# Kernel tuning notes

Hardware: AMD Instinct MI355X
Metric: run time of the kernel (lower is better)

Reference implementation:

```python
import jax, jax.numpy as jnp
import numpy as np

_EPS = 1e-08
SEG = 1024
HOP = 256
PAD = SEG // 2

# periodic Hann window, matching torch.hann_window(SEG) (periodic=True default)
_WINDOW = 0.5 * (1.0 - np.cos(2.0 * np.pi * np.arange(SEG) / SEG))


def setup_inputs() -> dict:
    key = jax.random.key(0)
    k1, k2 = jax.random.split(key)
    B, T = 32, 480000
    estimate = jax.random.normal(k1, (B, T), dtype=jnp.float32)
    target = jax.random.normal(k2, (B, T), dtype=jnp.float32)
    return {"estimate": estimate, "target": target}


def _frame(x):
    # x: [B, T_padded] -> [B, n_frames, SEG] overlapping frames (hop=HOP)
    n_frames = (x.shape[1] - SEG) // HOP + 1
    idx = np.arange(n_frames)[:, None] * HOP + np.arange(SEG)[None, :]
    return x[:, idx]


def reference(estimate, target):
    # zero-mean per utterance
    tgt = target - jnp.mean(target, axis=1, keepdims=True)
    est = estimate - jnp.mean(estimate, axis=1, keepdims=True)
    # centering: reflect-pad SEG//2 on both sides
    tgt = jnp.pad(tgt, ((0, 0), (PAD, PAD)), mode="reflect")
    est = jnp.pad(est, ((0, 0), (PAD, PAD)), mode="reflect")
    # overlapping frames + Hann windowing
    w = jnp.asarray(_WINDOW, dtype=tgt.dtype)  # [SEG]
    T_f = _frame(tgt) * w  # [B, F, SEG]
    E_f = _frame(est) * w  # [B, F, SEG]
    # SI-SDR per segment
    dot = jnp.sum(E_f * T_f, axis=2, keepdims=True)
    s_target_energy = jnp.sum(T_f * T_f, axis=2, keepdims=True) + _EPS
    scaled_target = dot * T_f / s_target_energy
    e_noise = E_f - scaled_target
    ratio = jnp.sum(scaled_target * scaled_target, axis=2) / (
        jnp.sum(e_noise * e_noise, axis=2) + _EPS
    )
    losses = -10.0 * jnp.log10(ratio + _EPS)  # [B, F]
    return losses
```

## Files before the change

kernel.cpp:

```cpp
#include <hip/hip_runtime.h>

#define NB 32
#define TLEN 480000
#define NF 1876
#define FR 4
#define WPR 469
#define WTHREADS 256

template <int CTRL>
__device__ __forceinline__ float dpp_add(float x) {
    int y = __builtin_amdgcn_update_dpp(0, __float_as_int(x), CTRL, 0xF, 0xF, true);
    return x + __int_as_float(y);
}

__device__ __forceinline__ float wave_reduce(float s) {
    s = dpp_add<0xB1>(s);
    s = dpp_add<0x4E>(s);
    s = dpp_add<0x124>(s);
    s = dpp_add<0x128>(s);
    s += __shfl_xor(s, 16);
    s += __shfl_xor(s, 32);
    return s;
}

__device__ __forceinline__ float f4c(const float4& v, int j) {
    return j == 0 ? v.x : (j == 1 ? v.y : (j == 2 ? v.z : v.w));
}

__device__ __forceinline__ float w2fast(float p) {
    float w = 0.5f - 0.5f * __cosf(p * (6.28318530717958647692f / 1024.0f));
    return w * w;
}

__global__ __launch_bounds__(WTHREADS) void seg_frames(
    const float* __restrict__ est, const float* __restrict__ tgt,
    float* __restrict__ ws_part, float* __restrict__ ws_bs)
{
    const int tid  = threadIdx.x;
    const int lane = tid & 63;
    const int wave = tid >> 6;
    const int b    = blockIdx.y;
    const int wv   = blockIdx.x * 4 + wave;
    if (wv >= WPR) return;
    const int fb = wv * FR;

    const float* erow = est + (size_t)b * TLEN;
    const float* trow = tgt + (size_t)b * TLEN;

    float pe = 0.f, pt = 0.f;

    if (fb >= 4 && fb <= 1868) {
        const float4* e4 = (const float4*)erow;
        const float4* t4 = (const float4*)trow;

        float4 E[7], T[7];
#pragma unroll
        for (int m = 0; m < 7; ++m) {
            int g = 64 * (fb + m) - 128 + lane;
            E[m] = e4[g];
            T[m] = t4[g];
        }

        float w2v[4][4];
#pragma unroll
        for (int q = 0; q < 4; ++q)
#pragma unroll
            for (int j = 0; j < 4; ++j)
                w2v[q][j] = w2fast((float)(256 * q + 4 * lane + j));

        float acc[4][5];
#pragma unroll
        for (int i = 0; i < 4; ++i)
#pragma unroll
            for (int s5 = 0; s5 < 5; ++s5) acc[i][s5] = 0.f;

#pragma unroll
        for (int m = 0; m < 7; ++m) {
            float4 ev4 = E[m], tv4 = T[m];
#pragma unroll
            for (int j = 0; j < 4; ++j) {
                float e = f4c(ev4, j), t = f4c(tv4, j);
                float et = e * t, tt2 = t * t, ee2 = e * e;
#pragma unroll
                for (int i = 0; i < 4; ++i) {
                    if (m - i < 0 || m - i > 3) continue;
                    float w2 = w2v[m - i][j];
                    acc[i][0] = fmaf(w2, et,  acc[i][0]);
                    acc[i][1] = fmaf(w2, tt2, acc[i][1]);
                    acc[i][2] = fmaf(w2, ee2, acc[i][2]);
                    acc[i][3] = fmaf(w2, e,   acc[i][3]);
                    acc[i][4] = fmaf(w2, t,   acc[i][4]);
                }
            }
            if (m < 4) {
                pe += (ev4.x + ev4.y) + (ev4.z + ev4.w);
                pt += (tv4.x + tv4.y) + (tv4.z + tv4.w);
            }
        }

#pragma unroll
        for (int i = 0; i < 4; ++i) {
            float s0 = wave_reduce(acc[i][0]);
            float s1 = wave_reduce(acc[i][1]);
            float s2 = wave_reduce(acc[i][2]);
            float s3 = wave_reduce(acc[i][3]);
            float s4 = wave_reduce(acc[i][4]);
            if (lane == 0) {
                float* p = ws_part + (size_t)(b * NF + fb + i) * 5;
                p[0] = s0; p[1] = s1; p[2] = s2; p[3] = s3; p[4] = s4;
            }
        }
    } else {
        int nfr = NF - fb;
        if (nfr > FR) nfr = FR;

        float w2v[4][4];
#pragma unroll
        for (int q = 0; q < 4; ++q)
#pragma unroll
            for (int j = 0; j < 4; ++j)
                w2v[q][j] = w2fast((float)(256 * q + 4 * lane + j));

        for (int i = 0; i < nfr; ++i) {
            int f = fb + i;
            float s_et = 0.f, s_tt = 0.f, s_ee = 0.f, s_e = 0.f, s_t = 0.f;
#pragma unroll
            for (int q = 0; q < 4; ++q)
#pragma unroll
                for (int j = 0; j < 4; ++j) {
                    int s = 256 * f - 512 + 256 * q + 4 * lane + j;
                    int idx = s < 0 ? -s : (s >= TLEN ? 2 * (TLEN - 1) - s : s);
                    float ev = erow[idx], tv = trow[idx];
                    float w2 = w2v[q][j];
                    float et = ev * tv;
                    s_et = fmaf(w2, et,      s_et);
                    s_tt = fmaf(w2, tv * tv, s_tt);
                    s_ee = fmaf(w2, ev * ev, s_ee);
                    s_e  = fmaf(w2, ev, s_e);
                    s_t  = fmaf(w2, tv, s_t);
                }
            s_et = wave_reduce(s_et);
            s_tt = wave_reduce(s_tt);
            s_ee = wave_reduce(s_ee);
            s_e  = wave_reduce(s_e);
            s_t  = wave_reduce(s_t);
            if (lane == 0) {
                float* p = ws_part + (size_t)(b * NF + f) * 5;
                p[0] = s_et; p[1] = s_tt; p[2] = s_ee; p[3] = s_e; p[4] = s_t;
            }
        }

        const float4* e4 = (const float4*)erow;
        const float4* t4 = (const float4*)trow;
        if (fb == 0) {
#pragma unroll
            for (int k = 0; k < 2; ++k) {
                float4 ev4 = e4[lane + 64 * k];
                float4 tv4 = t4[lane + 64 * k];
                pe += (ev4.x + ev4.y) + (ev4.z + ev4.w);
                pt += (tv4.x + tv4.y) + (tv4.z + tv4.w);
            }
        } else {
#pragma unroll
            for (int k = 0; k < 5; ++k) {
                int g = 119680 + lane + 64 * k;
                float4 ev4 = e4[g];
                float4 tv4 = t4[g];
                pe += (ev4.x + ev4.y) + (ev4.z + ev4.w);
                pt += (tv4.x + tv4.y) + (tv4.z + tv4.w);
            }
        }
    }

    pe = wave_reduce(pe);
    pt = wave_reduce(pt);
    if (lane == 0) {
        ws_bs[(0 * NB + b) * WPR + wv] = pe;
        ws_bs[(1 * NB + b) * WPR + wv] = pt;
    }
}

__global__ __launch_bounds__(WTHREADS) void seg_final(
    const float* __restrict__ ws_part, const float* __restrict__ ws_bs,
    float* __restrict__ out)
{
    const int tid  = threadIdx.x;
    const int lane = tid & 63;
    const int wave = tid >> 6;
    const int idx0 = blockIdx.x * WTHREADS;

    int b0 = idx0 / NF;
    int ilast = idx0 + WTHREADS - 1;
    if (ilast > NB * NF - 1) ilast = NB * NF - 1;
    int b1 = ilast / NF;

    __shared__ float smean[4];
    {
        int sig = wave & 1;
        int row = (wave >> 1) ? b1 : b0;
        const float* pbs = ws_bs + (size_t)(sig * NB + row) * WPR;
        float s = 0.f;
        for (int c = lane; c < WPR; c += 64) s += pbs[c];
        s = wave_reduce(s);
        if (lane == 0) smean[wave] = s * (1.0f / (float)TLEN);
    }
    __syncthreads();

    int idx = idx0 + tid;
    if (idx >= NB * NF) return;
    int b = idx / NF;
    int which = (b == b0) ? 0 : 1;
    float me = smean[which * 2 + 0];
    float mt = smean[which * 2 + 1];

    const float* p = ws_part + (size_t)idx * 5;
    float S_et = p[0], S_tt = p[1], S_ee = p[2], S_e = p[3], S_t = p[4];
    const float W2 = 384.0f;

    float dot = S_et - mt * S_e - me * S_t + me * mt * W2;
    float tt  = S_tt - 2.0f * mt * S_t + mt * mt * W2;
    float ee  = S_ee - 2.0f * me * S_e + me * me * W2;

    float a     = dot / (tt + 1e-8f);
    float st2   = a * a * tt;
    float en2   = ee - 2.0f * a * dot + st2;
    float ratio = st2 / (en2 + 1e-8f);
    out[idx] = -10.0f * log10f(ratio + 1e-8f);
}

extern "C" void kernel_launch(void* const* d_in, const int* in_sizes, int n_in,
                              void* d_out, int out_size, void* d_ws, size_t ws_size,
                              hipStream_t stream)
{
    const float* est = (const float*)d_in[0];
    const float* tgt = (const float*)d_in[1];
    float* out = (float*)d_out;

    float* ws      = (float*)d_ws;
    float* ws_part = ws;
    float* ws_bs   = ws_part + (size_t)NB * NF * 5;

    dim3 grid1((WPR + 3) / 4, NB);
    seg_frames<<<grid1, WTHREADS, 0, stream>>>(est, tgt, ws_part, ws_bs);
    dim3 grid2((NB * NF + WTHREADS - 1) / WTHREADS);
    seg_final<<<grid2, WTHREADS, 0, stream>>>(ws_part, ws_bs, out);
}
```

Measured before the change: 35.95 us.

## Widen each wave to a 16-frame strip with rolling register reuse

Each wave now computes 16 consecutive frames instead of 4, holding an 11-slot rolling register buffer of float4 chunks. Each group of 4 frames reuses 7 chunks, and later chunks are loaded into slots that are no longer needed. This cuts redundant global loads of overlapping frame data from 7/4 to about 19/16 chunks per frame. Results are packed across lanes so lanes 0-4 write all 16 frames' partial sums, and launch bounds request 2 blocks per SM. The trade-off is fewer waves (118 per row), so there is less parallelism and more register pressure, and edge strips now cover 16 frames on the slow reflect path.

Result: slower. 44.89 us (+24.9%).

```diff
diff --git a/kernel.cpp b/kernel.cpp
--- a/kernel.cpp
+++ b/kernel.cpp
@@ -3,8 +3,8 @@
 #define NB 32
 #define TLEN 480000
 #define NF 1876
-#define FR 4
-#define WPR 469
+#define FSTRIP 16
+#define WPR 118
 #define WTHREADS 256
 
 template <int CTRL>
@@ -32,7 +32,7 @@
     return w * w;
 }
 
-__global__ __launch_bounds__(WTHREADS) void seg_frames(
+__global__ __launch_bounds__(WTHREADS, 2) void seg_frames(
     const float* __restrict__ est, const float* __restrict__ tgt,
     float* __restrict__ ws_part, float* __restrict__ ws_bs)
 {
@@ -42,23 +42,23 @@
     const int b    = blockIdx.y;
     const int wv   = blockIdx.x * 4 + wave;
     if (wv >= WPR) return;
-    const int fb = wv * FR;
+    const int fb = wv * FSTRIP;
 
     const float* erow = est + (size_t)b * TLEN;
     const float* trow = tgt + (size_t)b * TLEN;
 
     float pe = 0.f, pt = 0.f;
 
-    if (fb >= 4 && fb <= 1868) {
+    if (wv >= 1 && wv <= 116) {
         const float4* e4 = (const float4*)erow;
         const float4* t4 = (const float4*)trow;
-
-        float4 E[7], T[7];
-#pragma unroll
-        for (int m = 0; m < 7; ++m) {
-            int g = 64 * (fb + m) - 128 + lane;
-            E[m] = e4[g];
-            T[m] = t4[g];
+        const int gbase = 1024 * wv - 128 + lane;
+
+        float4 E[11], T[11];
+#pragma unroll
+        for (int m = 0; m < 11; ++m) {
+            E[m] = e4[gbase + 64 * m];
+            T[m] = t4[gbase + 64 * m];
         }
 
         float w2v[4][4];
@@ -68,51 +68,81 @@
             for (int j = 0; j < 4; ++j)
                 w2v[q][j] = w2fast((float)(256 * q + 4 * lane + j));
 
-        float acc[4][5];
-#pragma unroll
-        for (int i = 0; i < 4; ++i)
-#pragma unroll
-            for (int s5 = 0; s5 < 5; ++s5) acc[i][s5] = 0.f;
-
-#pragma unroll
-        for (int m = 0; m < 7; ++m) {
-            float4 ev4 = E[m], tv4 = T[m];
-#pragma unroll
-            for (int j = 0; j < 4; ++j) {
-                float e = f4c(ev4, j), t = f4c(tv4, j);
-                float et = e * t, tt2 = t * t, ee2 = e * e;
-#pragma unroll
-                for (int i = 0; i < 4; ++i) {
-                    if (m - i < 0 || m - i > 3) continue;
-                    float w2 = w2v[m - i][j];
-                    acc[i][0] = fmaf(w2, et,  acc[i][0]);
-                    acc[i][1] = fmaf(w2, tt2, acc[i][1]);
-                    acc[i][2] = fmaf(w2, ee2, acc[i][2]);
-                    acc[i][3] = fmaf(w2, e,   acc[i][3]);
-                    acc[i][4] = fmaf(w2, t,   acc[i][4]);
-                }
-            }
-            if (m < 4) {
-                pe += (ev4.x + ev4.y) + (ev4.z + ev4.w);
-                pt += (tv4.x + tv4.y) + (tv4.z + tv4.w);
-            }
-        }
-
-#pragma unroll
-        for (int i = 0; i < 4; ++i) {
-            float s0 = wave_reduce(acc[i][0]);
-            float s1 = wave_reduce(acc[i][1]);
-            float s2 = wave_reduce(acc[i][2]);
-            float s3 = wave_reduce(acc[i][3]);
-            float s4 = wave_reduce(acc[i][4]);
-            if (lane == 0) {
-                float* p = ws_part + (size_t)(b * NF + fb + i) * 5;
-                p[0] = s0; p[1] = s1; p[2] = s2; p[3] = s3; p[4] = s4;
-            }
+        float vres[FSTRIP];
+
+#pragma unroll
+        for (int gq = 0; gq < 4; ++gq) {
+            if (gq == 1) {
+#pragma unroll
+                for (int m = 11; m < 15; ++m) {
+                    E[m - 11] = e4[gbase + 64 * m];
+                    T[m - 11] = t4[gbase + 64 * m];
+                }
+            }
+            if (gq == 2) {
+#pragma unroll
+                for (int m = 15; m < 19; ++m) {
+                    E[m - 11] = e4[gbase + 64 * m];
+                    T[m - 11] = t4[gbase + 64 * m];
+                }
+            }
+
+            float acc[4][5];
+#pragma unroll
+            for (int i = 0; i < 4; ++i)
+#pragma unroll
+                for (int s5 = 0; s5 < 5; ++s5) acc[i][s5] = 0.f;
+
+#pragma unroll
+            for (int k = 0; k < 7; ++k) {
+                const int slot = (4 * gq + k) % 11;
+                float4 ev4 = E[slot], tv4 = T[slot];
+#pragma unroll
+                for (int j = 0; j < 4; ++j) {
+                    float e = f4c(ev4, j), t = f4c(tv4, j);
+                    float et = e * t, tt2 = t * t, ee2 = e * e;
+#pragma unroll
+                    for (int i = 0; i < 4; ++i) {
+                        if (k - i < 0 || k - i > 3) continue;
+                        float w2 = w2v[k - i][j];
+                        acc[i][0] = fmaf(w2, et,  acc[i][0]);
+                        acc[i][1] = fmaf(w2, tt2, acc[i][1]);
+                        acc[i][2] = fmaf(w2, ee2, acc[i][2]);
+                        acc[i][3] = fmaf(w2, e,   acc[i][3]);
+                        acc[i][4] = fmaf(w2, t,   acc[i][4]);
+                    }
+                }
+                if (k >= 2 && k <= 5) {
+                    pe += (ev4.x + ev4.y) + (ev4.z + ev4.w);
+                    pt += (tv4.x + tv4.y) + (tv4.z + tv4.w);
+                }
+            }
+
+#pragma unroll
+            for (int i = 0; i < 4; ++i) {
+                float s0 = wave_reduce(acc[i][0]);
+                float s1 = wave_reduce(acc[i][1]);
+                float s2 = wave_reduce(acc[i][2]);
+                float s3 = wave_reduce(acc[i][3]);
+                float s4 = wave_reduce(acc[i][4]);
+                float v = s0;
+                v = (lane == 1) ? s1 : v;
+                v = (lane == 2) ? s2 : v;
+                v = (lane == 3) ? s3 : v;
+                v = (lane == 4) ? s4 : v;
+                vres[4 * gq + i] = v;
+            }
+        }
+
+        if (lane < 5) {
+            float* pbase = ws_part + (size_t)(b * NF + fb) * 5 + lane;
+#pragma unroll
+            for (int fi = 0; fi < FSTRIP; ++fi)
+                pbase[fi * 5] = vres[fi];
         }
     } else {
         int nfr = NF - fb;
-        if (nfr > FR) nfr = FR;
+        if (nfr > FSTRIP) nfr = FSTRIP;
 
         float w2v[4][4];
 #pragma unroll
@@ -154,7 +184,7 @@
         const float4* t4 = (const float4*)trow;
         if (fb == 0) {
 #pragma unroll
-            for (int k = 0; k < 2; ++k) {
+            for (int k = 0; k < 16; ++k) {
                 float4 ev4 = e4[lane + 64 * k];
                 float4 tv4 = t4[lane + 64 * k];
                 pe += (ev4.x + ev4.y) + (ev4.z + ev4.w);
@@ -162,8 +192,8 @@
             }
         } else {
 #pragma unroll
-            for (int k = 0; k < 5; ++k) {
-                int g = 119680 + lane + 64 * k;
+            for (int k = 0; k < 3; ++k) {
+                int g = 119808 + lane + 64 * k;
                 float4 ev4 = e4[g];
                 float4 tv4 = t4[g];
                 pe += (ev4.x + ev4.y) + (ev4.z + ev4.w);
```

## Stage per-block signal chunks in LDS via direct global-to-LDS loads

Applied to the files above, without the earlier changes.

Each block now covers a 16-frame chunk of one row. It loads the shared chunk plus halo once into LDS, using global_load_lds for interior chunks and a reflect-indexed scalar load at the edges, and then each wave computes 4 frames from LDS. Before, each wave loaded its own 7 float4 per lane straight from global memory, so neighbouring waves re-read the overlapping halo. This cuts redundant global traffic and unifies the boundary path, at the cost of a __syncthreads, LDS use, and a larger block-level mean-partial layout.

Measured after the change: 38.17 us. 6.2% more time.

```diff
diff --git a/kernel.cpp b/kernel.cpp
--- a/kernel.cpp
+++ b/kernel.cpp
@@ -1,10 +1,11 @@
 #include <hip/hip_runtime.h>
+#include <stdint.h>
 
 #define NB 32
 #define TLEN 480000
 #define NF 1876
-#define FR 4
-#define WPR 469
+#define NCH 118
+#define CH_F4 1216
 #define WTHREADS 256
 
 template <int CTRL>
@@ -32,35 +33,73 @@
     return w * w;
 }
 
+__device__ __forceinline__ void gl_lds16(const float4* gsrc, float4* ldst) {
+    auto lds = reinterpret_cast<__attribute__((address_space(3))) uint32_t*>(
+        reinterpret_cast<uintptr_t>(ldst));
+    auto g = reinterpret_cast<const __attribute__((address_space(1))) uint32_t*>(
+        reinterpret_cast<uintptr_t>(gsrc));
+    __builtin_amdgcn_global_load_lds(g, lds, 16, 0, 0);
+}
+
 __global__ __launch_bounds__(WTHREADS) void seg_frames(
     const float* __restrict__ est, const float* __restrict__ tgt,
     float* __restrict__ ws_part, float* __restrict__ ws_bs)
 {
+    __shared__ float4 se4[CH_F4];
+    __shared__ float4 st4[CH_F4];
+
     const int tid  = threadIdx.x;
     const int lane = tid & 63;
     const int wave = tid >> 6;
     const int b    = blockIdx.y;
-    const int wv   = blockIdx.x * 4 + wave;
-    if (wv >= WPR) return;
-    const int fb = wv * FR;
+    const int c    = blockIdx.x;
 
     const float* erow = est + (size_t)b * TLEN;
     const float* trow = tgt + (size_t)b * TLEN;
 
-    float pe = 0.f, pt = 0.f;
-
-    if (fb >= 4 && fb <= 1868) {
+    if (c >= 1 && c <= 116) {
         const float4* e4 = (const float4*)erow;
         const float4* t4 = (const float4*)trow;
-
-        float4 E[7], T[7];
-#pragma unroll
-        for (int m = 0; m < 7; ++m) {
-            int g = 64 * (fb + m) - 128 + lane;
-            E[m] = e4[g];
-            T[m] = t4[g];
-        }
-
+        const int g0 = 1024 * c - 128;
+#pragma unroll
+        for (int k = 0; k < 5; ++k) {
+            int vb = k * 256 + 64 * wave;
+            if (vb < CH_F4) {
+                gl_lds16(&e4[g0 + vb + lane], &se4[vb]);
+                gl_lds16(&t4[g0 + vb + lane], &st4[vb]);
+            }
+        }
+    } else {
+        float* se = (float*)se4;
+        float* st = (float*)st4;
+        for (int v = tid; v < 4 * CH_F4; v += WTHREADS) {
+            int s = 4096 * c - 512 + v;
+            int idx = s < 0 ? -s : (s >= TLEN ? 2 * (TLEN - 1) - s : s);
+            se[v] = erow[idx];
+            st[v] = trow[idx];
+        }
+    }
+    __syncthreads();
+
+    int owned = TLEN - 4096 * c;
+    if (owned > 4096) owned = 4096;
+    const int o4 = owned >> 2;
+    float pe = 0.f, pt = 0.f;
+    for (int u = tid; u < o4; u += WTHREADS) {
+        float4 ev = se4[128 + u], tv = st4[128 + u];
+        pe += (ev.x + ev.y) + (ev.z + ev.w);
+        pt += (tv.x + tv.y) + (tv.z + tv.w);
+    }
+    pe = wave_reduce(pe);
+    pt = wave_reduce(pt);
+    if (lane == 0) {
+        ws_bs[(0 * NB + b) * (NCH * 4) + c * 4 + wave] = pe;
+        ws_bs[(1 * NB + b) * (NCH * 4) + c * 4 + wave] = pt;
+    }
+
+    int nfr = NF - 16 * c;
+    if (nfr > 16) nfr = 16;
+    if (4 * wave < nfr) {
         float w2v[4][4];
 #pragma unroll
         for (int q = 0; q < 4; ++q)
@@ -76,7 +115,8 @@
 
 #pragma unroll
         for (int m = 0; m < 7; ++m) {
-            float4 ev4 = E[m], tv4 = T[m];
+            float4 ev4 = se4[256 * wave + 64 * m + lane];
+            float4 tv4 = st4[256 * wave + 64 * m + lane];
 #pragma unroll
             for (int j = 0; j < 4; ++j) {
                 float e = f4c(ev4, j), t = f4c(tv4, j);
@@ -92,91 +132,24 @@
                     acc[i][4] = fmaf(w2, t,   acc[i][4]);
                 }
             }
-            if (m < 4) {
-                pe += (ev4.x + ev4.y) + (ev4.z + ev4.w);
-                pt += (tv4.x + tv4.y) + (tv4.z + tv4.w);
+        }
+
+        const int f0 = 16 * c + 4 * wave;
+        const int nlocal = (nfr - 4 * wave < 4) ? (nfr - 4 * wave) : 4;
+#pragma unroll
+        for (int i = 0; i < 4; ++i) {
+            if (i < nlocal) {
+                float s0 = wave_reduce(acc[i][0]);
+                float s1 = wave_reduce(acc[i][1]);
+                float s2 = wave_reduce(acc[i][2]);
+                float s3 = wave_reduce(acc[i][3]);
+                float s4 = wave_reduce(acc[i][4]);
+                if (lane == 0) {
+                    float* p = ws_part + (size_t)(b * NF + f0 + i) * 5;
+                    p[0] = s0; p[1] = s1; p[2] = s2; p[3] = s3; p[4] = s4;
+                }
             }
         }
-
-#pragma unroll
-        for (int i = 0; i < 4; ++i) {
-            float s0 = wave_reduce(acc[i][0]);
-            float s1 = wave_reduce(acc[i][1]);
-            float s2 = wave_reduce(acc[i][2]);
-            float s3 = wave_reduce(acc[i][3]);
-            float s4 = wave_reduce(acc[i][4]);
-            if (lane == 0) {
-                float* p = ws_part + (size_t)(b * NF + fb + i) * 5;
-                p[0] = s0; p[1] = s1; p[2] = s2; p[3] = s3; p[4] = s4;
-            }
-        }
-    } else {
-        int nfr = NF - fb;
-        if (nfr > FR) nfr = FR;
-
-        float w2v[4][4];
-#pragma unroll
-        for (int q = 0; q < 4; ++q)
-#pragma unroll
-            for (int j = 0; j < 4; ++j)
-                w2v[q][j] = w2fast((float)(256 * q + 4 * lane + j));
-
-        for (int i = 0; i < nfr; ++i) {
-            int f = fb + i;
-            float s_et = 0.f, s_tt = 0.f, s_ee = 0.f, s_e = 0.f, s_t = 0.f;
-#pragma unroll
-            for (int q = 0; q < 4; ++q)
-#pragma unroll
-                for (int j = 0; j < 4; ++j) {
-                    int s = 256 * f - 512 + 256 * q + 4 * lane + j;
-                    int idx = s < 0 ? -s : (s >= TLEN ? 2 * (TLEN - 1) - s : s);
-                    float ev = erow[idx], tv = trow[idx];
-                    float w2 = w2v[q][j];
-                    float et = ev * tv;
-                    s_et = fmaf(w2, et,      s_et);
-                    s_tt = fmaf(w2, tv * tv, s_tt);
-                    s_ee = fmaf(w2, ev * ev, s_ee);
-                    s_e  = fmaf(w2, ev, s_e);
-                    s_t  = fmaf(w2, tv, s_t);
-                }
-            s_et = wave_reduce(s_et);
-            s_tt = wave_reduce(s_tt);
-            s_ee = wave_reduce(s_ee);
-            s_e  = wave_reduce(s_e);
-            s_t  = wave_reduce(s_t);
-            if (lane == 0) {
-                float* p = ws_part + (size_t)(b * NF + f) * 5;
-                p[0] = s_et; p[1] = s_tt; p[2] = s_ee; p[3] = s_e; p[4] = s_t;
-            }
-        }
-
-        const float4* e4 = (const float4*)erow;
-        const float4* t4 = (const float4*)trow;
-        if (fb == 0) {
-#pragma unroll
-            for (int k = 0; k < 2; ++k) {
-                float4 ev4 = e4[lane + 64 * k];
-                float4 tv4 = t4[lane + 64 * k];
-                pe += (ev4.x + ev4.y) + (ev4.z + ev4.w);
-                pt += (tv4.x + tv4.y) + (tv4.z + tv4.w);
-            }
-        } else {
-#pragma unroll
-            for (int k = 0; k < 5; ++k) {
-                int g = 119680 + lane + 64 * k;
-                float4 ev4 = e4[g];
-                float4 tv4 = t4[g];
-                pe += (ev4.x + ev4.y) + (ev4.z + ev4.w);
-                pt += (tv4.x + tv4.y) + (tv4.z + tv4.w);
-            }
-        }
-    }
-
-    pe = wave_reduce(pe);
-    pt = wave_reduce(pt);
-    if (lane == 0) {
-        ws_bs[(0 * NB + b) * WPR + wv] = pe;
-        ws_bs[(1 * NB + b) * WPR + wv] = pt;
     }
 }
 
@@ -198,9 +171,9 @@
     {
         int sig = wave & 1;
         int row = (wave >> 1) ? b1 : b0;
-        const float* pbs = ws_bs + (size_t)(sig * NB + row) * WPR;
+        const float* pbs = ws_bs + (size_t)(sig * NB + row) * (NCH * 4);
         float s = 0.f;
-        for (int c = lane; c < WPR; c += 64) s += pbs[c];
+        for (int u = lane; u < NCH * 4; u += 64) s += pbs[u];
         s = wave_reduce(s);
         if (lane == 0) smean[wave] = s * (1.0f / (float)TLEN);
     }
@@ -240,7 +213,7 @@
     float* ws_part = ws;
     float* ws_bs   = ws_part + (size_t)NB * NF * 5;
 
-    dim3 grid1((WPR + 3) / 4, NB);
+    dim3 grid1(NCH, NB);
     seg_frames<<<grid1, WTHREADS, 0, stream>>>(est, tgt, ws_part, ws_bs);
     dim3 grid2((NB * NF + WTHREADS - 1) / WTHREADS);
     seg_final<<<grid2, WTHREADS, 0, stream>>>(ws_part, ws_bs, out);
```
